# Kernel tuning notes

Hardware: AMD Instinct MI355X
Metric: run time of the kernel (lower is better)

The kernel has to match this reference:

```python
import jax, jax.numpy as jnp
import numpy as np

N_ATOMS = 1048576
N_CRYS = 8192
NFEA = 128
NCLS = 5
LN_EPS = 1e-5


def setup_inputs() -> dict:
    key = jax.random.key(0)
    k1, k2, k3 = jax.random.split(key, 3)
    data_crys_fea = jax.random.normal(k1, (N_ATOMS, NFEA), dtype=jnp.float32)
    # Contiguous non-empty [start, end) ranges partitioning [0, N_ATOMS)
    rng = np.random.default_rng(0)
    cuts = np.sort(rng.choice(np.arange(1, N_ATOMS), size=N_CRYS - 1, replace=False))
    starts = np.concatenate([[0], cuts])
    ends = np.concatenate([cuts, [N_ATOMS]])
    data_crys_idx = jnp.asarray(np.stack([starts, ends], axis=1).astype(np.int32))
    ln_weight = jnp.ones((NFEA,), dtype=jnp.float32)
    ln_bias = jnp.zeros((NFEA,), dtype=jnp.float32)
    out_w = jax.random.normal(k2, (NCLS, NFEA), dtype=jnp.float32) / np.sqrt(NFEA).astype(np.float32)
    out_b = jax.random.normal(k3, (NCLS,), dtype=jnp.float32) * 0.01
    return {
        "data_crys_fea": data_crys_fea,
        "data_crys_idx": data_crys_idx,
        "ln_weight": ln_weight,
        "ln_bias": ln_bias,
        "out_w": out_w,
        "out_b": out_b,
    }


def reference(data_crys_fea, data_crys_idx, ln_weight, ln_bias, out_w, out_b):
    # --- pool: per-crystal mean over contiguous [start, end) atom ranges ---
    starts = data_crys_idx[:, 0]
    ends = data_crys_idx[:, 1]
    n_atoms = data_crys_fea.shape[0]
    # segment id of each atom via searchsorted on sorted starts
    seg = jnp.searchsorted(starts, jnp.arange(n_atoms, dtype=starts.dtype), side="right") - 1
    seg_sum = jax.ops.segment_sum(data_crys_fea, seg, num_segments=N_CRYS)  # [n_crys, F]
    lens = (ends - starts).astype(data_crys_fea.dtype)
    pooled = seg_sum / lens[:, None]
    # --- LayerNorm over features (biased variance, eps=1e-5, like torch) ---
    mu = jnp.mean(pooled, axis=-1, keepdims=True)
    var = jnp.var(pooled, axis=-1, keepdims=True)
    normed = (pooled - mu) / jnp.sqrt(var + LN_EPS) * ln_weight + ln_bias
    # --- Softplus then Linear ---
    act = jax.nn.softplus(normed)  # [n_crys, F]
    my_output = act @ out_w.T + out_b  # [n_crys, n_cls]
    return my_output, act
```

## Files before the change

### kernel.cpp

```cpp
#include <hip/hip_runtime.h>
#include <hip/hip_bf16.h>

#define NFEA 128
#define NCLS 5
#define LN_EPS 1e-5f
#define SLAB 128

typedef float f32x4 __attribute__((ext_vector_type(4)));

__device__ __forceinline__ void finalize_vec(
    int lane, int fc, int c, f32x4 sum, float inv_len,
    const float* __restrict__ lnw, const float* __restrict__ lnb,
    const float* __restrict__ outw, const float* __restrict__ outb,
    float* __restrict__ out_cls, float* __restrict__ out_act)
{
    f32x4 p;
    p[0] = sum[0] * inv_len; p[1] = sum[1] * inv_len;
    p[2] = sum[2] * inv_len; p[3] = sum[3] * inv_len;

    float t = p[0] + p[1] + p[2] + p[3];
    #pragma unroll
    for (int off = 16; off; off >>= 1) t += __shfl_xor(t, off);
    const float mu = t * (1.f / NFEA);

    f32x4 d;
    d[0] = p[0] - mu; d[1] = p[1] - mu; d[2] = p[2] - mu; d[3] = p[3] - mu;
    float v = d[0]*d[0] + d[1]*d[1] + d[2]*d[2] + d[3]*d[3];
    #pragma unroll
    for (int off = 16; off; off >>= 1) v += __shfl_xor(v, off);
    const float rstd = rsqrtf(v * (1.f / NFEA) + LN_EPS);

    const f32x4 w4 = ((const f32x4*)lnw)[fc];
    const f32x4 b4 = ((const f32x4*)lnb)[fc];
    f32x4 act;
    #pragma unroll
    for (int j = 0; j < 4; ++j) {
        const float x = d[j] * rstd * w4[j] + b4[j];
        act[j] = (x > 0.f) ? x + log1pf(expf(-x)) : log1pf(expf(x));
    }
    if (lane < 32) ((f32x4*)out_act)[(size_t)c * 32 + fc] = act;

    #pragma unroll
    for (int k = 0; k < NCLS; ++k) {
        const f32x4 wk = ((const f32x4*)outw)[k * 32 + fc];
        float pk = act[0]*wk[0] + act[1]*wk[1] + act[2]*wk[2] + act[3]*wk[3];
        #pragma unroll
        for (int off = 16; off; off >>= 1) pk += __shfl_xor(pk, off);
        if (lane == k) out_cls[(size_t)c * NCLS + k] = pk + outb[k];
    }
}

__global__ __launch_bounds__(256) void prep_kernel(
    const int2* __restrict__ idx,
    int*  __restrict__ seg_of_slab,
    float* __restrict__ seg_sum,
    int n_crys)
{
    const int t    = blockIdx.x * 256 + threadIdx.x;
    const int nthr = gridDim.x * 256;

    f32x4* z = (f32x4*)seg_sum;
    const int nz = n_crys * NFEA / 4;
    for (int i = t; i < nz; i += nthr) z[i] = (f32x4){0.f, 0.f, 0.f, 0.f};

    if (t < n_crys) {
        const int2 se = idx[t];
        int j = (se.x + SLAB - 1) / SLAB;
        for (; j * SLAB < se.y; ++j) seg_of_slab[j] = t;
    }
}

__global__ __launch_bounds__(256) void main_kernel(
    const float* __restrict__ fea,
    const int2*  __restrict__ idx,
    const int*   __restrict__ seg_of_slab,
    float* __restrict__ seg_sum,
    const float* __restrict__ lnw, const float* __restrict__ lnb,
    const float* __restrict__ outw, const float* __restrict__ outb,
    float* __restrict__ out_cls, float* __restrict__ out_act)
{
    const int gw   = (blockIdx.x * 256 + threadIdx.x) >> 6;
    const int lane = threadIdx.x & 63;
    const int fc   = lane & 31;
    const int al   = lane >> 5;
    const int a0   = gw * SLAB;
    const int a1   = a0 + SLAB;

    int s = seg_of_slab[gw];
    const f32x4* __restrict__ fea4 = (const f32x4*)fea;

    int rs = a0;
    while (rs < a1) {
        const int2 se = idx[s];
        const int re = min(se.y, a1);

        f32x4 acc0 = {0.f,0.f,0.f,0.f};
        f32x4 acc1 = {0.f,0.f,0.f,0.f};
        f32x4 acc2 = {0.f,0.f,0.f,0.f};
        f32x4 acc3 = {0.f,0.f,0.f,0.f};

        int a = rs + al;
        if (a + 6 < re) {
            f32x4 v0 = __builtin_nontemporal_load(fea4 + (size_t)a       * 32 + fc);
            f32x4 v1 = __builtin_nontemporal_load(fea4 + (size_t)(a + 2) * 32 + fc);
            f32x4 v2 = __builtin_nontemporal_load(fea4 + (size_t)(a + 4) * 32 + fc);
            f32x4 v3 = __builtin_nontemporal_load(fea4 + (size_t)(a + 6) * 32 + fc);
            a += 8;
            for (; a + 6 < re; a += 8) {
                f32x4 n0 = __builtin_nontemporal_load(fea4 + (size_t)a       * 32 + fc);
                f32x4 n1 = __builtin_nontemporal_load(fea4 + (size_t)(a + 2) * 32 + fc);
                f32x4 n2 = __builtin_nontemporal_load(fea4 + (size_t)(a + 4) * 32 + fc);
                f32x4 n3 = __builtin_nontemporal_load(fea4 + (size_t)(a + 6) * 32 + fc);
                acc0 += v0; acc1 += v1; acc2 += v2; acc3 += v3;
                v0 = n0; v1 = n1; v2 = n2; v3 = n3;
            }
            acc0 += v0; acc1 += v1; acc2 += v2; acc3 += v3;
        }
        for (; a < re; a += 2)
            acc0 += __builtin_nontemporal_load(fea4 + (size_t)a * 32 + fc);

        f32x4 accT = acc0 + acc1;
        accT += acc2; accT += acc3;

        accT[0] += __shfl_xor(accT[0], 32);
        accT[1] += __shfl_xor(accT[1], 32);
        accT[2] += __shfl_xor(accT[2], 32);
        accT[3] += __shfl_xor(accT[3], 32);

        const bool interior = (se.x >= a0) && (se.y <= a1);
        if (interior) {
            finalize_vec(lane, fc, s, accT, 1.f / (float)(se.y - se.x),
                         lnw, lnb, outw, outb, out_cls, out_act);
        } else if (lane < 32) {
            float* dst = &seg_sum[(size_t)s * NFEA + fc * 4];
            atomicAdd(dst + 0, accT[0]);
            atomicAdd(dst + 1, accT[1]);
            atomicAdd(dst + 2, accT[2]);
            atomicAdd(dst + 3, accT[3]);
        }
        rs = re; ++s;
    }
}

__global__ __launch_bounds__(256) void cleanup_kernel(
    const float* __restrict__ seg_sum,
    const int2*  __restrict__ idx,
    const float* __restrict__ lnw, const float* __restrict__ lnb,
    const float* __restrict__ outw, const float* __restrict__ outb,
    float* __restrict__ out_cls, float* __restrict__ out_act,
    int n_crys)
{
    const int c    = (blockIdx.x * 256 + threadIdx.x) >> 6;
    const int lane = threadIdx.x & 63;
    if (c >= n_crys) return;
    const int2 se = idx[c];
    if ((se.x / SLAB) == ((se.y - 1) / SLAB)) return;

    const int fc = lane & 31;
    const f32x4 sum = ((const f32x4*)seg_sum)[(size_t)c * 32 + fc];
    finalize_vec(lane, fc, c, sum, 1.f / (float)(se.y - se.x),
                 lnw, lnb, outw, outb, out_cls, out_act);
}

extern "C" void kernel_launch(void* const* d_in, const int* in_sizes, int n_in,
                              void* d_out, int out_size, void* d_ws, size_t ws_size,
                              hipStream_t stream) {
    const float* fea  = (const float*)d_in[0];
    const int2*  idx  = (const int2*)d_in[1];
    const float* lnw  = (const float*)d_in[2];
    const float* lnb  = (const float*)d_in[3];
    const float* outw = (const float*)d_in[4];
    const float* outb = (const float*)d_in[5];

    const int n_crys  = in_sizes[1] / 2;
    const int n_atoms = in_sizes[0] / NFEA;
    const int nslab   = n_atoms / SLAB;

    float* seg_sum     = (float*)d_ws;
    int*   seg_of_slab = (int*)((char*)d_ws + (size_t)n_crys * NFEA * sizeof(float));

    float* out_cls = (float*)d_out;
    float* out_act = (float*)d_out + (size_t)n_crys * NCLS;

    prep_kernel<<<256, 256, 0, stream>>>(idx, seg_of_slab, seg_sum, n_crys);
    main_kernel<<<nslab / 4, 256, 0, stream>>>(fea, idx, seg_of_slab, seg_sum,
                                               lnw, lnb, outw, outb, out_cls, out_act);
    cleanup_kernel<<<(n_crys + 3) / 4, 256, 0, stream>>>(seg_sum, idx, lnw, lnb,
                                                         outw, outb, out_cls, out_act,
                                                         n_crys);
}
```

Measured before the change: 140.6 us.

## Switch to block-per-chunk segment sums with shared-memory reduction and separate finalize

Each 256-thread block now handles a 256-atom chunk instead of each wave handling a 128-atom slab. Partial sums are reduced across the block's 8 row groups in shared memory, and every segment, interior ones included, is atomically accumulated into global seg_sum. All LayerNorm, softplus and linear work moves to a separate finalize kernel. Nontemporal loads are replaced by plain loads. This simplifies the main loop but adds two block barriers per segment, more atomics, and a second full pass over seg_sum in the finalize kernel.

```diff
diff --git a/kernel.cpp b/kernel.cpp
--- a/kernel.cpp
+++ b/kernel.cpp
@@ -4,7 +4,7 @@
 #define NFEA 128
 #define NCLS 5
 #define LN_EPS 1e-5f
-#define SLAB 128
+#define CHUNK 256
 
 typedef float f32x4 __attribute__((ext_vector_type(4)));
 
@@ -52,7 +52,7 @@
 
 __global__ __launch_bounds__(256) void prep_kernel(
     const int2* __restrict__ idx,
-    int*  __restrict__ seg_of_slab,
+    int*  __restrict__ seg_of_chunk,
     float* __restrict__ seg_sum,
     int n_crys)
 {
@@ -65,34 +65,30 @@
 
     if (t < n_crys) {
         const int2 se = idx[t];
-        int j = (se.x + SLAB - 1) / SLAB;
-        for (; j * SLAB < se.y; ++j) seg_of_slab[j] = t;
+        int j = (se.x + CHUNK - 1) / CHUNK;
+        for (; j * CHUNK < se.y; ++j) seg_of_chunk[j] = t;
     }
 }
 
-__global__ __launch_bounds__(256) void main_kernel(
+__global__ __launch_bounds__(256) void seg_sum_kernel(
     const float* __restrict__ fea,
     const int2*  __restrict__ idx,
-    const int*   __restrict__ seg_of_slab,
-    float* __restrict__ seg_sum,
-    const float* __restrict__ lnw, const float* __restrict__ lnb,
-    const float* __restrict__ outw, const float* __restrict__ outb,
-    float* __restrict__ out_cls, float* __restrict__ out_act)
+    const int*   __restrict__ seg_of_chunk,
+    float* __restrict__ seg_sum)
 {
-    const int gw   = (blockIdx.x * 256 + threadIdx.x) >> 6;
-    const int lane = threadIdx.x & 63;
-    const int fc   = lane & 31;
-    const int al   = lane >> 5;
-    const int a0   = gw * SLAB;
-    const int a1   = a0 + SLAB;
+    const int c0 = blockIdx.x * CHUNK;
+    const int c1 = c0 + CHUNK;
+    const int tid = threadIdx.x;
+    const int fc  = tid & 31;
+    const int al  = tid >> 5;
 
-    int s = seg_of_slab[gw];
+    int s = seg_of_chunk[blockIdx.x];
     const f32x4* __restrict__ fea4 = (const f32x4*)fea;
+    __shared__ f32x4 red4[8][32];
 
-    int rs = a0;
-    while (rs < a1) {
-        const int2 se = idx[s];
-        const int re = min(se.y, a1);
+    int rs = c0;
+    while (rs < c1) {
+        const int re = min(idx[s].y, c1);
 
         f32x4 acc0 = {0.f,0.f,0.f,0.f};
         f32x4 acc1 = {0.f,0.f,0.f,0.f};
@@ -100,49 +96,42 @@
         f32x4 acc3 = {0.f,0.f,0.f,0.f};
 
         int a = rs + al;
-        if (a + 6 < re) {
-            f32x4 v0 = __builtin_nontemporal_load(fea4 + (size_t)a       * 32 + fc);
-            f32x4 v1 = __builtin_nontemporal_load(fea4 + (size_t)(a + 2) * 32 + fc);
-            f32x4 v2 = __builtin_nontemporal_load(fea4 + (size_t)(a + 4) * 32 + fc);
-            f32x4 v3 = __builtin_nontemporal_load(fea4 + (size_t)(a + 6) * 32 + fc);
-            a += 8;
-            for (; a + 6 < re; a += 8) {
-                f32x4 n0 = __builtin_nontemporal_load(fea4 + (size_t)a       * 32 + fc);
-                f32x4 n1 = __builtin_nontemporal_load(fea4 + (size_t)(a + 2) * 32 + fc);
-                f32x4 n2 = __builtin_nontemporal_load(fea4 + (size_t)(a + 4) * 32 + fc);
-                f32x4 n3 = __builtin_nontemporal_load(fea4 + (size_t)(a + 6) * 32 + fc);
+        if (a + 24 < re) {
+            f32x4 v0 = fea4[(size_t)a        * 32 + fc];
+            f32x4 v1 = fea4[(size_t)(a + 8)  * 32 + fc];
+            f32x4 v2 = fea4[(size_t)(a + 16) * 32 + fc];
+            f32x4 v3 = fea4[(size_t)(a + 24) * 32 + fc];
+            a += 32;
+            for (; a + 24 < re; a += 32) {
+                f32x4 n0 = fea4[(size_t)a        * 32 + fc];
+                f32x4 n1 = fea4[(size_t)(a + 8)  * 32 + fc];
+                f32x4 n2 = fea4[(size_t)(a + 16) * 32 + fc];
+                f32x4 n3 = fea4[(size_t)(a + 24) * 32 + fc];
                 acc0 += v0; acc1 += v1; acc2 += v2; acc3 += v3;
                 v0 = n0; v1 = n1; v2 = n2; v3 = n3;
             }
             acc0 += v0; acc1 += v1; acc2 += v2; acc3 += v3;
         }
-        for (; a < re; a += 2)
-            acc0 += __builtin_nontemporal_load(fea4 + (size_t)a * 32 + fc);
+        for (; a < re; a += 8)
+            acc0 += fea4[(size_t)a * 32 + fc];
 
-        f32x4 accT = acc0 + acc1;
-        accT += acc2; accT += acc3;
+        f32x4 accT = (acc0 + acc1) + (acc2 + acc3);
 
-        accT[0] += __shfl_xor(accT[0], 32);
-        accT[1] += __shfl_xor(accT[1], 32);
-        accT[2] += __shfl_xor(accT[2], 32);
-        accT[3] += __shfl_xor(accT[3], 32);
-
-        const bool interior = (se.x >= a0) && (se.y <= a1);
-        if (interior) {
-            finalize_vec(lane, fc, s, accT, 1.f / (float)(se.y - se.x),
-                         lnw, lnb, outw, outb, out_cls, out_act);
-        } else if (lane < 32) {
-            float* dst = &seg_sum[(size_t)s * NFEA + fc * 4];
-            atomicAdd(dst + 0, accT[0]);
-            atomicAdd(dst + 1, accT[1]);
-            atomicAdd(dst + 2, accT[2]);
-            atomicAdd(dst + 3, accT[3]);
+        red4[al][fc] = accT;
+        __syncthreads();
+        if (tid < NFEA) {
+            const float* redf = (const float*)red4;
+            float ssum = 0.f;
+            #pragma unroll
+            for (int g = 0; g < 8; ++g) ssum += redf[g * NFEA + tid];
+            atomicAdd(&seg_sum[(size_t)s * NFEA + tid], ssum);
         }
+        __syncthreads();
         rs = re; ++s;
     }
 }
 
-__global__ __launch_bounds__(256) void cleanup_kernel(
+__global__ __launch_bounds__(256) void finalize_kernel(
     const float* __restrict__ seg_sum,
     const int2*  __restrict__ idx,
     const float* __restrict__ lnw, const float* __restrict__ lnb,
@@ -154,8 +143,6 @@
     const int lane = threadIdx.x & 63;
     if (c >= n_crys) return;
     const int2 se = idx[c];
-    if ((se.x / SLAB) == ((se.y - 1) / SLAB)) return;
-
     const int fc = lane & 31;
     const f32x4 sum = ((const f32x4*)seg_sum)[(size_t)c * 32 + fc];
     finalize_vec(lane, fc, c, sum, 1.f / (float)(se.y - se.x),
@@ -174,18 +161,16 @@
 
     const int n_crys  = in_sizes[1] / 2;
     const int n_atoms = in_sizes[0] / NFEA;
-    const int nslab   = n_atoms / SLAB;
+    const int nchunk  = n_atoms / CHUNK;
 
-    float* seg_sum     = (float*)d_ws;
-    int*   seg_of_slab = (int*)((char*)d_ws + (size_t)n_crys * NFEA * sizeof(float));
+    float* seg_sum      = (float*)d_ws;
+    int*   seg_of_chunk = (int*)((char*)d_ws + (size_t)n_crys * NFEA * sizeof(float));
 
     float* out_cls = (float*)d_out;
     float* out_act = (float*)d_out + (size_t)n_crys * NCLS;
 
-    prep_kernel<<<256, 256, 0, stream>>>(idx, seg_of_slab, seg_sum, n_crys);
-    main_kernel<<<nslab / 4, 256, 0, stream>>>(fea, idx, seg_of_slab, seg_sum,
-                                               lnw, lnb, outw, outb, out_cls, out_act);
-    cleanup_kernel<<<(n_crys + 3) / 4, 256, 0, stream>>>(seg_sum, idx, lnw, lnb,
-                                                         outw, outb, out_cls, out_act,
-                                                         n_crys);
+    prep_kernel<<<256, 256, 0, stream>>>(idx, seg_of_chunk, seg_sum, n_crys);
+    seg_sum_kernel<<<nchunk, 256, 0, stream>>>(fea, idx, seg_of_chunk, seg_sum);
+    finalize_kernel<<<(n_crys + 3) / 4, 256, 0, stream>>>(
+        seg_sum, idx, lnw, lnb, outw, outb, out_cls, out_act, n_crys);
 }
```

Measured after the change: 133.3 us. 5.2% less time.
